# Kernel optimization log

Hardware: AMD Instinct MI355X
Metric: run time of the kernel (lower is better)

The kernel has to match this reference:

```python
import jax, jax.numpy as jnp
import numpy as np

B, S, U, H = 32, 8192, 1024, 1024


def setup_inputs() -> dict:
    key = jax.random.key(0)
    k1, k2, k3, k4, k5 = jax.random.split(key, 5)
    inp = jax.random.randint(k1, (B, S, H), -128, 128, dtype=jnp.int32).astype(jnp.int8)
    indices = jax.random.randint(k2, (B,), 0, S - U + 1, dtype=jnp.int32)
    updates = jax.random.normal(k3, (B, U, H), dtype=jnp.float16)
    # scales strictly positive, bounded away from zero
    quant_scales = jax.random.uniform(k4, (H,), dtype=jnp.float32, minval=0.01, maxval=1.0)
    quant_zero_points = jax.random.normal(k5, (H,), dtype=jnp.float32)
    return {
        "input": inp,
        "indices": indices,
        "updates": updates,
        "quant_scales": quant_scales,
        "quant_zero_points": quant_zero_points,
        "axis": 1,
    }


def _quantize(updates, quant_scales, quant_zero_points):
    u = updates.astype(jnp.float32)
    # scales / zero-points broadcast from trailing dims (left-unsqueeze semantics)
    q = jnp.round(u / quant_scales + quant_zero_points)
    q = jnp.clip(q, -128.0, 127.0)
    q = jnp.where(jnp.isneginf(u), -128.0, q)
    q = jnp.where(jnp.isposinf(u), 127.0, q)
    return q.astype(jnp.int8)


def reference(input, indices, updates, quant_scales, quant_zero_points, axis):
    if axis < 0:
        axis = input.ndim + axis
    q = _quantize(updates, quant_scales, quant_zero_points)
    # move scatter axis next to batch axis for a single vectorized scatter
    qm = jnp.moveaxis(q, axis, 1)            # [B, U, ...]
    outm = jnp.moveaxis(input, axis, 1)      # [B, S, ...]
    upd_len = qm.shape[1]
    b = jnp.arange(qm.shape[0])[:, None]                         # [B, 1]
    pos = indices.astype(jnp.int64)[:, None] + jnp.arange(upd_len)[None, :]  # [B, U]
    outm = outm.at[b, pos].set(qm)
    return jnp.moveaxis(outm, 1, axis)
```

## Files before the change

### kernel.cpp

```cpp
#include <hip/hip_runtime.h>


typedef float f32x4 __attribute__((ext_vector_type(4)));
typedef int   i32x4 __attribute__((ext_vector_type(4)));

#define BB 32
#define SS 8192
#define UU 1024
#define HH 1024

__device__ __forceinline__ int quant1(float u, float r, float z) {
    float q = rintf(fmaf(u, r, z));
    q = fminf(fmaxf(q, -128.0f), 127.0f);
    return (int)q;
}

__global__ __launch_bounds__(256) void scatter_quant_kernel(
        const int* __restrict__ inp,
        const int* __restrict__ idxs,
        const float* __restrict__ upd,
        const float* __restrict__ scales,
        const float* __restrict__ zps,
        int* __restrict__ out) {
    const int tid     = (int)blockIdx.x * 256 + (int)threadIdx.x;
    const int h       = (tid & 255) << 2;
    const int rowslot = tid >> 8;

    const f32x4 sc = *reinterpret_cast<const f32x4*>(scales + h);
    const f32x4 zp = *reinterpret_cast<const f32x4*>(zps + h);
    const f32x4 rc = { 1.0f / sc.x, 1.0f / sc.y, 1.0f / sc.z, 1.0f / sc.w };

    for (int b = 0; b < BB; ++b) {
        const int idx = idxs[b];
        const long long bbase = ((long long)b << 23) + h;
        const float* updb = upd + (((long long)b) << 20) + h;

#pragma unroll 1
        for (int t = 0; t < 4; ++t) {
            const int s = (t << 11) + rowslot;
            const unsigned urow = (unsigned)(s - idx);
            const long long off = bbase + ((long long)s << 10);

            i32x4 o;
            if (urow < (unsigned)UU) {
                const f32x4 u = *reinterpret_cast<const f32x4*>(
                    updb + ((long long)urow << 10));
                o.x = quant1(u.x, rc.x, zp.x);
                o.y = quant1(u.y, rc.y, zp.y);
                o.z = quant1(u.z, rc.z, zp.z);
                o.w = quant1(u.w, rc.w, zp.w);
            } else {
                o = *reinterpret_cast<const i32x4*>(inp + off);
            }
            *reinterpret_cast<i32x4*>(out + off) = o;
        }
    }
}

extern "C" void kernel_launch(void* const* d_in, const int* in_sizes, int n_in,
                              void* d_out, int out_size, void* d_ws, size_t ws_size,
                              hipStream_t stream) {
    const int*   inp    = (const int*)d_in[0];
    const int*   idxs   = (const int*)d_in[1];
    const float* upd    = (const float*)d_in[2];
    const float* scales = (const float*)d_in[3];
    const float* zps    = (const float*)d_in[4];
    int*         out    = (int*)d_out;

    scatter_quant_kernel<<<2048, 256, 0, stream>>>(inp, idxs, upd, scales, zps, out);
}
```

Measured before the change: 447.1 us.

## Split grid into dedicated copy blocks and quantize-scatter blocks

Partitions the grid so that most blocks copy only rows outside the update window, remapping logical rows past the window. The remaining blocks each quantize a chunk of one batch's updates straight into the window. This removes the per-row branch between copy and quantize paths and makes each block's access pattern uniform. It relies on the launch grid matching the hardcoded block counts.

```diff
diff --git a/kernel.cpp b/kernel.cpp
--- a/kernel.cpp
+++ b/kernel.cpp
@@ -8,6 +8,8 @@
 #define SS 8192
 #define UU 1024
 #define HH 1024
+#define NB1 1792
+#define ROWS_NU 7168
 
 __device__ __forceinline__ int quant1(float u, float r, float z) {
     float q = rintf(fmaf(u, r, z));
@@ -22,37 +24,42 @@
         const float* __restrict__ scales,
         const float* __restrict__ zps,
         int* __restrict__ out) {
-    const int tid     = (int)blockIdx.x * 256 + (int)threadIdx.x;
-    const int h       = (tid & 255) << 2;
-    const int rowslot = tid >> 8;
+    const int g        = (int)blockIdx.x;
+    const int lane_off = (int)threadIdx.x << 2;
 
-    const f32x4 sc = *reinterpret_cast<const f32x4*>(scales + h);
-    const f32x4 zp = *reinterpret_cast<const f32x4*>(zps + h);
-    const f32x4 rc = { 1.0f / sc.x, 1.0f / sc.y, 1.0f / sc.z, 1.0f / sc.w };
+    if (g < NB1) {
+        for (int t = 0; t < 128; ++t) {
+            const int b   = t >> 2;
+            const int idx = idxs[b];
+            const int r   = (t & 3) * NB1 + g;
+            const int phys = r + (r >= idx ? UU : 0);
+            const long long e = ((((long long)b << 13) + phys) << 10) + lane_off;
+            *reinterpret_cast<i32x4*>(out + e) =
+                *reinterpret_cast<const i32x4*>(inp + e);
+        }
+    } else {
+        const int k   = g - NB1;
+        const int b   = k >> 3;
+        const int sub = k & 7;
+        const int idx = idxs[b];
 
-    for (int b = 0; b < BB; ++b) {
-        const int idx = idxs[b];
-        const long long bbase = ((long long)b << 23) + h;
-        const float* updb = upd + (((long long)b) << 20) + h;
+        const f32x4 sc = *reinterpret_cast<const f32x4*>(scales + lane_off);
+        const f32x4 zp = *reinterpret_cast<const f32x4*>(zps + lane_off);
+        const f32x4 rc = { 1.0f / sc.x, 1.0f / sc.y, 1.0f / sc.z, 1.0f / sc.w };
 
-#pragma unroll 1
-        for (int t = 0; t < 4; ++t) {
-            const int s = (t << 11) + rowslot;
-            const unsigned urow = (unsigned)(s - idx);
-            const long long off = bbase + ((long long)s << 10);
+        const float* updb = upd + ((long long)b << 20) + lane_off;
+        int* outb = out + ((((long long)b << 13) + idx) << 10) + lane_off;
 
-            i32x4 o;
-            if (urow < (unsigned)UU) {
-                const f32x4 u = *reinterpret_cast<const f32x4*>(
-                    updb + ((long long)urow << 10));
-                o.x = quant1(u.x, rc.x, zp.x);
-                o.y = quant1(u.y, rc.y, zp.y);
-                o.z = quant1(u.z, rc.z, zp.z);
-                o.w = quant1(u.w, rc.w, zp.w);
-            } else {
-                o = *reinterpret_cast<const i32x4*>(inp + off);
-            }
-            *reinterpret_cast<i32x4*>(out + off) = o;
+        for (int t = 0; t < 128; ++t) {
+            const int u = (sub << 7) + t;
+            const f32x4 v = *reinterpret_cast<const f32x4*>(
+                updb + ((long long)u << 10));
+            i32x4 q;
+            q.x = quant1(v.x, rc.x, zp.x);
+            q.y = quant1(v.y, rc.y, zp.y);
+            q.z = quant1(v.z, rc.z, zp.z);
+            q.w = quant1(v.w, rc.w, zp.w);
+            *reinterpret_cast<i32x4*>(outb + ((long long)u << 10)) = q;
         }
     }
 }
```

After: 433.9 us. -3.0%, faster.
